# Optimization experiments

Measured on AMD Instinct MI355X. Metric: run time of the kernel, lower is better.

The kernel has to match this reference:

```python
import jax, jax.numpy as jnp
import numpy as np
import math

B, SEQ_LEN, ENC_IN = 8, 1021, 12
D_MODEL, N_HEADS, D_FF, E_LAYERS = 512, 8, 2048, 3
FACTOR, NUM_CLASS = 5, 10
BN_EPS = 1e-5


def _pos_encoding(L, d):
    pos = np.arange(L, dtype=np.float32)[:, None]
    div = np.exp(np.arange(0, d, 2, dtype=np.float32) * (-math.log(10000.0) / d))
    pe = np.zeros((L, d), dtype=np.float32)
    pe[:, 0::2] = np.sin(pos * div)
    pe[:, 1::2] = np.cos(pos * div)
    return jnp.asarray(pe)


def _layer_norm(x, w, b, eps=1e-5):
    mu = jnp.mean(x, -1, keepdims=True)
    var = jnp.mean((x - mu) ** 2, -1, keepdims=True)
    return (x - mu) * jax.lax.rsqrt(var + eps) * w + b


def _circ_conv1d(x, w, b=None):
    # x: [B,C,L], w: [O,C,3]; circular pad 1 each side then valid conv (torch padding_mode='circular')
    xp = jnp.concatenate([x[..., -1:], x, x[..., :1]], axis=-1)
    y = jax.lax.conv_general_dilated(xp, w, (1,), 'VALID', dimension_numbers=('NCH', 'OIH', 'NCH'))
    return y if b is None else y + b[None, :, None]


def _prob_attention(q, k, v, rng):
    # ProbSparse attention (mask_flag=False). q,k,v: [B,H,L,Dh]
    Bq, H, L, Dh = q.shape
    n = min(FACTOR * int(math.ceil(math.log(L))), L)      # U_part == u (L_Q == L_K)
    idx = jax.random.randint(rng, (L, n), 0, L)           # sampled key ids per query
    k_sample = k[:, :, idx, :]                            # [B,H,L,n,Dh]
    qk_sample = jnp.einsum('bhld,bhlsd->bhls', q, k_sample)
    m = qk_sample.max(-1) - qk_sample.sum(-1) / L         # sparsity measure M
    _, m_top = jax.lax.top_k(m, n)                        # [B,H,n] active queries
    q_red = jnp.take_along_axis(q, m_top[..., None], axis=2)   # [B,H,n,Dh]
    scores = jnp.einsum('bhud,bhld->bhul', q_red, k) * (1.0 / math.sqrt(Dh))
    attn = jax.nn.softmax(scores, axis=-1)
    upd = jnp.einsum('bhul,bhld->bhud', attn, v)          # [B,H,n,Dh]
    ctx = jnp.broadcast_to(jnp.mean(v, axis=2, keepdims=True), (Bq, H, L, Dh))  # initial context = mean(V)
    b_ix = jnp.arange(Bq)[:, None, None]
    h_ix = jnp.arange(H)[None, :, None]
    ctx = ctx.at[b_ix, h_ix, m_top].set(upd)
    return jnp.transpose(ctx, (0, 2, 1, 3))               # [B,L,H,Dh]


def _encoder_layer(x, l, attn_wq, attn_bq, attn_wk, attn_bk, attn_wv, attn_bv,
                   attn_wo, attn_bo, ln1_w, ln1_b, ln2_w, ln2_b,
                   ff1_w, ff1_b, ff2_w, ff2_b, rng):
    Bx, L, dm = x.shape
    Dh = dm // N_HEADS
    q = (x @ attn_wq[l].T + attn_bq[l]).reshape(Bx, L, N_HEADS, Dh).transpose(0, 2, 1, 3)
    k = (x @ attn_wk[l].T + attn_bk[l]).reshape(Bx, L, N_HEADS, Dh).transpose(0, 2, 1, 3)
    v = (x @ attn_wv[l].T + attn_bv[l]).reshape(Bx, L, N_HEADS, Dh).transpose(0, 2, 1, 3)
    ctx = _prob_attention(q, k, v, rng).reshape(Bx, L, dm)
    new_x = ctx @ attn_wo[l].T + attn_bo[l]
    x = _layer_norm(x + new_x, ln1_w[l], ln1_b[l])
    y = jax.nn.gelu(x @ ff1_w[l].T + ff1_b[l], approximate=False)
    y = y @ ff2_w[l].T + ff2_b[l]
    return _layer_norm(x + y, ln2_w[l], ln2_b[l])


def _conv_layer(x, cw, cb, bnw, bnb):
    # distillation: circular conv -> BatchNorm (eval, mean 0 / var 1) -> ELU -> MaxPool(3,2,pad=1)
    h = _circ_conv1d(jnp.transpose(x, (0, 2, 1)), cw, cb)
    h = h * (bnw * (1.0 / math.sqrt(1.0 + BN_EPS)))[None, :, None] + bnb[None, :, None]
    h = jax.nn.elu(h)
    h = jax.lax.reduce_window(h, -np.inf, jax.lax.max, (1, 1, 3), (1, 1, 2),
                              ((0, 0), (0, 0), (1, 1)))
    return jnp.transpose(h, (0, 2, 1))


def _forward(x_enc, tok_w, attn_wq, attn_bq, attn_wk, attn_bk, attn_wv, attn_bv,
             attn_wo, attn_bo, ln1_w, ln1_b, ln2_w, ln2_b, ff1_w, ff1_b, ff2_w, ff2_b,
             cv_w, cv_b, bn_w, bn_b, norm_w, norm_b, proj_w, proj_b):
    rngs = jax.random.split(jax.random.key(42), E_LAYERS)
    # DataEmbedding = TokenEmbedding (circular conv, no bias) + sinusoidal positional
    x = jnp.transpose(_circ_conv1d(jnp.transpose(x_enc, (0, 2, 1)), tok_w), (0, 2, 1))
    x = x + _pos_encoding(x.shape[1], D_MODEL)[None]
    for l in range(E_LAYERS):
        x = _encoder_layer(x, l, attn_wq, attn_bq, attn_wk, attn_bk, attn_wv, attn_bv,
                           attn_wo, attn_bo, ln1_w, ln1_b, ln2_w, ln2_b,
                           ff1_w, ff1_b, ff2_w, ff2_b, rngs[l])
        if l < E_LAYERS - 1:
            x = _conv_layer(x, cv_w[l], cv_b[l], bn_w[l], bn_b[l])
    x = _layer_norm(x, norm_w, norm_b)
    out = jax.nn.gelu(x, approximate=False)
    out = out.reshape(out.shape[0], -1)    # [B, d_model * conv_seq_len]
    return out @ proj_w.T + proj_b


def setup_inputs() -> dict:
    key = jax.random.key(0)
    ks = jax.random.split(key, 32)
    d, ff = D_MODEL, D_FF

    def nrm(k, shape, scale=1.0):
        return jax.random.normal(k, shape, dtype=jnp.float32) * scale

    s_d = 1.0 / math.sqrt(d)
    return {
        'x_enc': nrm(ks[0], (B, SEQ_LEN, ENC_IN)),
        'tok_w': nrm(ks[1], (d, ENC_IN, 3), 1.0 / math.sqrt(ENC_IN * 3)),
        'attn_wq': nrm(ks[2], (E_LAYERS, d, d), s_d), 'attn_bq': nrm(ks[3], (E_LAYERS, d), 0.02),
        'attn_wk': nrm(ks[4], (E_LAYERS, d, d), s_d), 'attn_bk': nrm(ks[5], (E_LAYERS, d), 0.02),
        'attn_wv': nrm(ks[6], (E_LAYERS, d, d), s_d), 'attn_bv': nrm(ks[7], (E_LAYERS, d), 0.02),
        'attn_wo': nrm(ks[8], (E_LAYERS, d, d), s_d), 'attn_bo': nrm(ks[9], (E_LAYERS, d), 0.02),
        'ln1_w': jnp.ones((E_LAYERS, d), jnp.float32), 'ln1_b': jnp.zeros((E_LAYERS, d), jnp.float32),
        'ln2_w': jnp.ones((E_LAYERS, d), jnp.float32), 'ln2_b': jnp.zeros((E_LAYERS, d), jnp.float32),
        'ff1_w': nrm(ks[10], (E_LAYERS, ff, d), s_d), 'ff1_b': nrm(ks[11], (E_LAYERS, ff), 0.02),
        'ff2_w': nrm(ks[12], (E_LAYERS, d, ff), 1.0 / math.sqrt(ff)), 'ff2_b': nrm(ks[13], (E_LAYERS, d), 0.02),
        'cv_w': nrm(ks[14], (E_LAYERS - 1, d, d, 3), 1.0 / math.sqrt(3 * d)),
        'cv_b': nrm(ks[15], (E_LAYERS - 1, d), 0.02),
        'bn_w': jnp.ones((E_LAYERS - 1, d), jnp.float32), 'bn_b': jnp.zeros((E_LAYERS - 1, d), jnp.float32),
        'norm_w': jnp.ones((d,), jnp.float32), 'norm_b': jnp.zeros((d,), jnp.float32),
        'proj_w': nrm(ks[16], (NUM_CLASS, d * 256), 1.0 / math.sqrt(d * 256)),
        'proj_b': jnp.zeros((NUM_CLASS,), jnp.float32),
    }


def reference(x_enc, tok_w, attn_wq, attn_bq, attn_wk, attn_bk, attn_wv, attn_bv,
              attn_wo, attn_bo, ln1_w, ln1_b, ln2_w, ln2_b, ff1_w, ff1_b, ff2_w, ff2_b,
              cv_w, cv_b, bn_w, bn_b, norm_w, norm_b, proj_w, proj_b):
    return _forward(x_enc, tok_w, attn_wq, attn_bq, attn_wk, attn_bk, attn_wv, attn_bv,
                    attn_wo, attn_bo, ln1_w, ln1_b, ln2_w, ln2_b, ff1_w, ff1_b, ff2_w, ff2_b,
                    cv_w, cv_b, bn_w, bn_b, norm_w, norm_b, proj_w, proj_b)
```

## Files before the change

kernel.cpp:

```cpp
#include <hip/hip_runtime.h>
#include <math.h>
#include <stdint.h>

typedef __attribute__((ext_vector_type(8))) short bf16x8;
typedef __attribute__((ext_vector_type(4))) float f32x4;

__device__ __forceinline__ unsigned short f2bf(float f){
  unsigned int u = __float_as_uint(f);
  unsigned int r = (u + 0x7fffu + ((u>>16)&1u)) >> 16;
  return (unsigned short)r;
}
__device__ __forceinline__ float bf2f(unsigned short h){
  return __uint_as_float(((unsigned int)h)<<16);
}
__device__ __forceinline__ void gload16(const void* g, void* l){
  __builtin_amdgcn_global_load_lds(
      (const __attribute__((address_space(1))) unsigned int*)g,
      (__attribute__((address_space(3))) unsigned int*)l, 16, 0, 0);
}

__host__ __device__ static inline uint32_t rotl32(uint32_t x, int d){ return (x<<d)|(x>>(32-d)); }
__host__ __device__ static inline void tf2x32(uint32_t k0, uint32_t k1, uint32_t c0, uint32_t c1,
                                              uint32_t* o0, uint32_t* o1){
  uint32_t ks0=k0, ks1=k1, ks2=k0^k1^0x1BD11BDAu;
  uint32_t x0=c0+ks0, x1=c1+ks1;
  const int ra[4]={13,15,26,6}, rb[4]={17,29,16,24};
  #pragma unroll
  for(int i=0;i<4;i++){x0+=x1;x1=rotl32(x1,ra[i]);x1^=x0;}
  x0+=ks1; x1+=ks2+1u;
  #pragma unroll
  for(int i=0;i<4;i++){x0+=x1;x1=rotl32(x1,rb[i]);x1^=x0;}
  x0+=ks2; x1+=ks0+2u;
  #pragma unroll
  for(int i=0;i<4;i++){x0+=x1;x1=rotl32(x1,ra[i]);x1^=x0;}
  x0+=ks0; x1+=ks1+3u;
  #pragma unroll
  for(int i=0;i<4;i++){x0+=x1;x1=rotl32(x1,rb[i]);x1^=x0;}
  x0+=ks1; x1+=ks2+4u;
  #pragma unroll
  for(int i=0;i<4;i++){x0+=x1;x1=rotl32(x1,ra[i]);x1^=x0;}
  x0+=ks2; x1+=ks0+5u;
  *o0=x0; *o1=x1;
}

__global__ __launch_bounds__(256) void gen_idx_k(uint32_t k1a,uint32_t k1b,
                                                 uint32_t k2a,uint32_t k2b,
                                                 int size,uint32_t span,uint32_t mult,
                                                 int* __restrict__ idx){
  int i = blockIdx.x*256 + threadIdx.x;
  if (i >= size) return;
  uint32_t h0,h1,l0,l1;
  tf2x32(k1a,k1b,0u,(uint32_t)i,&h0,&h1);
  tf2x32(k2a,k2b,0u,(uint32_t)i,&l0,&l1);
  uint32_t hb = h0^h1, lb = l0^l1;
  idx[i] = (int)((((hb%span)*mult) + (lb%span)) % span);
}

__global__ __launch_bounds__(256) void embed_k(const float* __restrict__ xe,
                                               const float* __restrict__ tw,
                                               float* __restrict__ X,
                                               short* __restrict__ Xh){
  int i = blockIdx.x*256 + threadIdx.x;
  int c = i & 511;
  int bl = i >> 9;
  int l = bl % 1021;
  int b = bl / 1021;
  float acc = 0.f;
  #pragma unroll
  for (int t=0;t<3;t++){
    int ls = l - 1 + t;
    ls = (ls < 0) ? 1020 : (ls >= 1021 ? 0 : ls);
    const float* xp = xe + (size_t)(b*1021 + ls)*12;
    const float* wp = tw + (size_t)c*36 + t;
    #pragma unroll
    for (int ci=0; ci<12; ci++) acc += xp[ci] * wp[ci*3];
  }
  int ip = c >> 1;
  float div = expf((float)(2*ip) * (float)(-9.210340371976184/512.0));
  float ang = (float)l * div;
  acc += (c & 1) ? cosf(ang) : sinf(ang);
  X[i] = acc;
  Xh[i] = f2bf(acc);
}

__global__ __launch_bounds__(256) void wcvt_k(const float* __restrict__ src,
                                              short* __restrict__ dst, int n){
  int i = blockIdx.x*256 + threadIdx.x;
  if (i < n) dst[i] = f2bf(src[i]);
}
__global__ __launch_bounds__(256) void convw_k(const float* __restrict__ cw,
                                               short* __restrict__ W){
  int i = blockIdx.x*256 + threadIdx.x;
  int col = i % 1536; int co = i / 1536;
  int t = col / 512; int ci = col % 512;
  W[i] = f2bf(cw[(size_t)co*1536 + ci*3 + t]);
}

__global__ __launch_bounds__(256) void gemm_bf16_k(
    const short* __restrict__ A, long Ab,
    const short* __restrict__ W, long Wb,
    const float* __restrict__ bias,
    float* __restrict__ Cf, short* __restrict__ Ch, long Cb,
    int M, int Nreal, int Nstride, int K, int mode,
    const float* __restrict__ s2, const float* __restrict__ b2,
    const float* __restrict__ rs, long rsb)
{
  __shared__ short As[4096];
  __shared__ short Bs[4096];
  const int t = threadIdx.x;
  const int lane = t & 63;
  const int w = t >> 6;
  const int wr = w >> 1, wc = w & 1;
  const int z = blockIdx.z;
  const int m0 = blockIdx.x * 128, n0 = blockIdx.y * 128;
  const short* Az = A + (size_t)z * Ab;
  const short* Wz = W + (size_t)z * Wb;

  f32x4 acc[4][4];
  #pragma unroll
  for (int i=0;i<4;i++)
    #pragma unroll
    for (int j=0;j<4;j++) acc[i][j] = (f32x4){0.f,0.f,0.f,0.f};

  const int r0  = t >> 2;
  const int k80 = (t & 3) << 3;
  char* AsB = (char*)As;
  char* BsB = (char*)Bs;

  for (int k0 = 0; k0 < K; k0 += 32){
    gload16(Az + (size_t)(m0 + r0)      * K + k0 + k80, AsB + (size_t)w*1024);
    gload16(Az + (size_t)(m0 + r0 + 64) * K + k0 + k80, AsB + 4096 + (size_t)w*1024);
    gload16(Wz + (size_t)(n0 + r0)      * K + k0 + k80, BsB + (size_t)w*1024);
    gload16(Wz + (size_t)(n0 + r0 + 64) * K + k0 + k80, BsB + 4096 + (size_t)w*1024);
    __syncthreads();
    bf16x8 a[4], b[4];
    #pragma unroll
    for (int mi=0; mi<4; mi++){
      int aoff = (wr*64 + mi*16 + (lane&15))*32 + ((lane>>4)<<3);
      a[mi] = *(const bf16x8*)(&As[aoff]);
    }
    #pragma unroll
    for (int ni=0; ni<4; ni++){
      int boff = (wc*64 + ni*16 + (lane&15))*32 + ((lane>>4)<<3);
      b[ni] = *(const bf16x8*)(&Bs[boff]);
    }
    #pragma unroll
    for (int mi=0; mi<4; mi++)
      #pragma unroll
      for (int ni=0; ni<4; ni++)
        acc[mi][ni] = __builtin_amdgcn_mfma_f32_16x16x32_bf16(a[mi], b[ni], acc[mi][ni], 0, 0, 0);
    __syncthreads();
  }

  #pragma unroll
  for (int mi=0; mi<4; mi++){
    #pragma unroll
    for (int r=0; r<4; r++){
      int gm = m0 + wr*64 + mi*16 + ((lane>>4)<<2) + r;
      if (gm >= M) continue;
      float rsc = (mode==4) ? rs[(size_t)z*rsb + gm] : 0.f;
      #pragma unroll
      for (int ni=0; ni<4; ni++){
        int gn = n0 + wc*64 + ni*16 + (lane&15);
        if (gn >= Nreal) continue;
        float v = acc[mi][ni][r];
        if (mode <= 2) v += bias[gn];
        if (mode == 1){
          v = 0.5f*v*(1.0f + erff(v*0.707106781186547524f));
        } else if (mode == 2){
          v = v * (s2[gn]*0.9999950000374997f) + b2[gn];
          v = (v > 0.f) ? v : expm1f(v);
        } else if (mode == 4){
          v *= rsc;
        }
        size_t off = (size_t)z*Cb + (size_t)gm*Nstride + gn;
        if (Cf) Cf[off] = v;
        if (Ch) Ch[off] = f2bf(v);
      }
    }
  }
}

__global__ __launch_bounds__(256) void qk_dot_k(const float* __restrict__ Q,
                                                const float* __restrict__ Kb,
                                                const int* __restrict__ idx,
                                                float* __restrict__ QK, int L, int n){
  long gi = (long)blockIdx.x*256 + threadIdx.x;
  long total = (long)64*L*n;
  if (gi >= total) return;
  int s = (int)(gi % n); long t2 = gi / n;
  int l = (int)(t2 % L); int bh = (int)(t2 / L);
  int h = bh & 7, b = bh >> 3;
  const float4* qp = (const float4*)(Q + (size_t)(b*L + l)*512 + h*64);
  int kr = idx[l*n + s];
  const float4* kp = (const float4*)(Kb + (size_t)(b*L + kr)*512 + h*64);
  float dot = 0.f;
  #pragma unroll
  for (int i=0;i<16;i++){
    float4 a = qp[i], c = kp[i];
    dot += a.x*c.x + a.y*c.y + a.z*c.z + a.w*c.w;
  }
  QK[gi] = dot;
}

__global__ __launch_bounds__(256) void reduce_m_k(const float* __restrict__ QK,
                                                  float* __restrict__ Mout, int L, int n){
  int gi = blockIdx.x*256 + threadIdx.x;
  if (gi >= 64*L) return;
  int l = gi % L; int bh = gi / L;
  const float* row = QK + (size_t)gi*n;
  float mx = -INFINITY, sm = 0.f;
  for (int s=0;s<n;s++){ float v = row[s]; mx = fmaxf(mx, v); sm += v; }
  Mout[(size_t)bh*1024 + l] = mx - sm/(float)L;
}

__global__ __launch_bounds__(64) void topk_k(const float* __restrict__ Mv,
                                             int* __restrict__ topk, int L, int n){
  int bh = blockIdx.x; int lane = threadIdx.x;
  float v[16];
  #pragma unroll
  for (int i=0;i<16;i++){ int l = i*64 + lane; v[i] = (l<L) ? Mv[(size_t)bh*1024 + l] : -INFINITY; }
  for (int it=0; it<n; ++it){
    float bv = -INFINITY; int bi = 0x7fffffff;
    #pragma unroll
    for (int i=0;i<16;i++){ int l = i*64+lane; if (v[i] > bv){ bv = v[i]; bi = l; } }
    #pragma unroll
    for (int o=32;o>0;o>>=1){
      float ov = __shfl_xor(bv, o); int oi = __shfl_xor(bi, o);
      if (ov > bv || (ov == bv && oi < bi)){ bv = ov; bi = oi; }
    }
    if (lane == 0) topk[bh*n + it] = bi;
    int wl = bi & 63, wi = bi >> 6;
    if (lane == wl){
      #pragma unroll
      for (int i=0;i<16;i++) if (i == wi) v[i] = -INFINITY;
    }
  }
}

__global__ __launch_bounds__(64) void qred_k(const float* __restrict__ Q,
                                             const int* __restrict__ topk,
                                             short* __restrict__ Qrh, int L, int n){
  int u = blockIdx.x % n; int bh = blockIdx.x / n;
  int h = bh & 7, b = bh >> 3; int d = threadIdx.x;
  int lq = topk[bh*n + u];
  Qrh[(size_t)bh*8192 + u*64 + d] = f2bf(0.125f * Q[(size_t)(b*L + lq)*512 + h*64 + d]);
}

__global__ __launch_bounds__(256) void kh_k(const float* __restrict__ Kb,
                                            short* __restrict__ Kh, int L){
  int i = blockIdx.x*256 + threadIdx.x;
  int d = i & 63; int l = (i>>6) & 1023; int bh = i >> 16;
  int h = bh & 7, b = bh >> 3;
  Kh[i] = (l < L) ? f2bf(Kb[(size_t)(b*L + l)*512 + h*64 + d]) : (short)0;
}

__global__ __launch_bounds__(256) void vt_k(const float* __restrict__ V,
                                            short* __restrict__ Vt, int L){
  __shared__ float ts[64][65];
  int z = blockIdx.x >> 4;
  int l0 = (blockIdx.x & 15) * 64;
  int h = z & 7, b = z >> 3;
  int t = threadIdx.x;
  for (int i = t; i < 4096; i += 256){
    int lloc = i >> 6, d = i & 63;
    int l = l0 + lloc;
    ts[d][lloc] = (l < L) ? V[(size_t)(b*L + l)*512 + h*64 + d] : 0.f;
  }
  __syncthreads();
  for (int i = t; i < 4096; i += 256){
    int d = i >> 6, lloc = i & 63;
    Vt[(size_t)z*131072 + (size_t)d*1024 + l0 + lloc] = f2bf(ts[d][lloc]);
  }
}

__global__ __launch_bounds__(256) void softmax_k(const float* __restrict__ S,
                                                 short* __restrict__ Ph,
                                                 float* __restrict__ RS, int L, int n){
  int u = blockIdx.x % n; int z = blockIdx.x / n;
  const float* srow = S + (size_t)z*n*1024 + (size_t)u*1024;
  short* prow = Ph + (size_t)z*131072 + (size_t)u*1024;
  int t = threadIdx.x;
  __shared__ float red[256];
  float lm = -INFINITY;
  for (int l=t; l<L; l+=256) lm = fmaxf(lm, srow[l]);
  red[t]=lm; __syncthreads();
  for (int o=128;o>0;o>>=1){ if(t<o) red[t]=fmaxf(red[t],red[t+o]); __syncthreads(); }
  float mx = red[0]; __syncthreads();
  float ls = 0.f;
  for (int l=t; l<1024; l+=256){
    float p = (l < L) ? expf(srow[l]-mx) : 0.f;
    prow[l] = f2bf(p);
    ls += p;
  }
  red[t]=ls; __syncthreads();
  for (int o=128;o>0;o>>=1){ if(t<o) red[t]+=red[t+o]; __syncthreads(); }
  if (t==0) RS[(size_t)z*n + u] = 1.0f/red[0];
}

__global__ __launch_bounds__(512) void vmean_part_k(const float* __restrict__ V,
                                                    float* __restrict__ part, int L){
  int b = blockIdx.x; int j = blockIdx.y; int c = threadIdx.x;
  float s = 0.f;
  for (int l = j; l < L; l += 16) s += V[(size_t)(b*L + l)*512 + c];
  part[(size_t)(b*16 + j)*512 + c] = s;
}
__global__ __launch_bounds__(256) void vmean_comb_k(const float* __restrict__ part,
                                                    float* __restrict__ vmean, int L){
  int i = blockIdx.x*256 + threadIdx.x;
  int b = i >> 9; int c = i & 511;
  float s = 0.f;
  #pragma unroll
  for (int j=0;j<16;j++) s += part[(size_t)(b*16 + j)*512 + c];
  vmean[i] = s / (float)L;
}
__global__ __launch_bounds__(256) void ctx_fill_k(short* __restrict__ CTXh,
                                                  const float* __restrict__ vmean, int L){
  int i = blockIdx.x*256 + threadIdx.x;
  int c = i & 511; int bl = i >> 9; int b = bl / L;
  CTXh[i] = f2bf(vmean[b*512 + c]);
}
__global__ __launch_bounds__(256) void ctx_scatter_k(short* __restrict__ CTXh,
                                                     const float* __restrict__ UPD,
                                                     const int* __restrict__ topk, int L, int n){
  int i = blockIdx.x*256 + threadIdx.x;
  int d = i & 63; int u = (i >> 6) % n; int bh = i / (64*n);
  int h = bh & 7; int b = bh >> 3;
  int lq = topk[bh*n + u];
  CTXh[(size_t)(b*L + lq)*512 + h*64 + d] = f2bf(UPD[((size_t)bh*n + u)*64 + d]);
}

__global__ __launch_bounds__(256) void add_ln_k(float* __restrict__ X,
                                                short* __restrict__ Xh,
                                                const float* __restrict__ Y,
                                                const float* __restrict__ w,
                                                const float* __restrict__ b){
  int r = blockIdx.x;
  size_t base = (size_t)r*512;
  int t = threadIdx.x;
  float v0 = X[base+t]     + Y[base+t];
  float v1 = X[base+t+256] + Y[base+t+256];
  __shared__ float red[256];
  red[t] = v0 + v1; __syncthreads();
  for (int o=128;o>0;o>>=1){ if(t<o) red[t]+=red[t+o]; __syncthreads(); }
  float mu = red[0]*(1.f/512.f); __syncthreads();
  float d0 = v0-mu, d1 = v1-mu;
  red[t] = d0*d0 + d1*d1; __syncthreads();
  for (int o=128;o>0;o>>=1){ if(t<o) red[t]+=red[t+o]; __syncthreads(); }
  float rs = 1.0f/sqrtf(red[0]*(1.f/512.f) + 1e-5f);
  float x0 = d0*rs*w[t]     + b[t];
  float x1 = d1*rs*w[t+256] + b[t+256];
  X[base+t]     = x0;  Xh[base+t]     = f2bf(x0);
  X[base+t+256] = x1;  Xh[base+t+256] = f2bf(x1);
}

__global__ __launch_bounds__(256) void ln_gelu_k(const float* __restrict__ X,
                                                 float* __restrict__ Yout,
                                                 const float* __restrict__ w,
                                                 const float* __restrict__ b){
  int r = blockIdx.x;
  size_t base = (size_t)r*512;
  int t = threadIdx.x;
  float v0 = X[base+t];
  float v1 = X[base+t+256];
  __shared__ float red[256];
  red[t] = v0 + v1; __syncthreads();
  for (int o=128;o>0;o>>=1){ if(t<o) red[t]+=red[t+o]; __syncthreads(); }
  float mu = red[0]*(1.f/512.f); __syncthreads();
  float d0 = v0-mu, d1 = v1-mu;
  red[t] = d0*d0 + d1*d1; __syncthreads();
  for (int o=128;o>0;o>>=1){ if(t<o) red[t]+=red[t+o]; __syncthreads(); }
  float rs = 1.0f/sqrtf(red[0]*(1.f/512.f) + 1e-5f);
  float g0 = d0*rs*w[t]     + b[t];
  float g1 = d1*rs*w[t+256] + b[t+256];
  Yout[base+t]     = 0.5f*g0*(1.0f + erff(g0*0.707106781186547524f));
  Yout[base+t+256] = 0.5f*g1*(1.0f + erff(g1*0.707106781186547524f));
}

__global__ __launch_bounds__(256) void im2col_k(const float* __restrict__ X,
                                                short* __restrict__ O, int L){
  int i = blockIdx.x*256 + threadIdx.x;
  int col = i % 1536; int bl = i / 1536;
  int l = bl % L; int b = bl / L;
  int t = col / 512; int ci = col % 512;
  int ls = l - 1 + t;
  ls = (ls < 0) ? (L-1) : (ls >= L ? 0 : ls);
  O[(size_t)bl*1536 + col] = f2bf(X[(size_t)(b*L + ls)*512 + ci]);
}
__global__ __launch_bounds__(256) void pool_k(const short* __restrict__ Hc,
                                              float* __restrict__ X,
                                              short* __restrict__ Xh, int L, int Lo){
  int i = blockIdx.x*256 + threadIdx.x;
  int c = i & 511; int r = i >> 9; int lo = r % Lo; int b = r / Lo;
  float m = -INFINITY;
  #pragma unroll
  for (int dt=-1; dt<=1; dt++){
    int li = 2*lo + dt;
    if (li >= 0 && li < L) m = fmaxf(m, bf2f((unsigned short)Hc[(size_t)(b*L + li)*512 + c]));
  }
  size_t o = (size_t)(b*Lo + lo)*512 + c;
  X[o] = m; Xh[o] = f2bf(m);
}

__global__ __launch_bounds__(256) void proj_part_k(const float* __restrict__ Xg,
                                                   const float* __restrict__ pw,
                                                   float* __restrict__ part){
  int b = blockIdx.x >> 5;
  int c = blockIdx.x & 31;
  int t = threadIdx.x;
  const float4* xp = (const float4*)(Xg + (size_t)b*131072 + (size_t)c*4096);
  float4 x0 = xp[t], x1 = xp[t+256], x2 = xp[t+512], x3 = xp[t+768];
  float acc[10];
  #pragma unroll
  for (int j=0;j<10;j++){
    const float4* wp = (const float4*)(pw + (size_t)j*131072 + (size_t)c*4096);
    float4 w0 = wp[t], w1 = wp[t+256], w2 = wp[t+512], w3 = wp[t+768];
    acc[j] = x0.x*w0.x + x0.y*w0.y + x0.z*w0.z + x0.w*w0.w
           + x1.x*w1.x + x1.y*w1.y + x1.z*w1.z + x1.w*w1.w
           + x2.x*w2.x + x2.y*w2.y + x2.z*w2.z + x2.w*w2.w
           + x3.x*w3.x + x3.y*w3.y + x3.z*w3.z + x3.w*w3.w;
  }
  __shared__ float red[256];
  #pragma unroll
  for (int j=0;j<10;j++){
    red[t] = acc[j]; __syncthreads();
    for (int o=128;o>0;o>>=1){ if(t<o) red[t]+=red[t+o]; __syncthreads(); }
    if (t==0) part[(b*10 + j)*32 + c] = red[0];
    __syncthreads();
  }
}
__global__ __launch_bounds__(128) void proj_comb_k(const float* __restrict__ part,
                                                   const float* __restrict__ pb,
                                                   float* __restrict__ out){
  int t = threadIdx.x;
  if (t >= 80) return;
  int j = t % 10;
  const float* p = part + t*32;
  float s = 0.f;
  #pragma unroll
  for (int c=0;c<32;c++) s += p[c];
  out[t] = s + pb[j];
}

extern "C" void kernel_launch(void* const* d_in, const int* in_sizes, int n_in,
                              void* d_out, int out_size, void* d_ws, size_t ws_size,
                              hipStream_t stream){
  (void)in_sizes; (void)n_in; (void)out_size; (void)ws_size;
  const float* x_enc = (const float*)d_in[0];
  const float* tok_w = (const float*)d_in[1];
  const float* wq    = (const float*)d_in[2];
  const float* bq    = (const float*)d_in[3];
  const float* wk    = (const float*)d_in[4];
  const float* bk    = (const float*)d_in[5];
  const float* wvp   = (const float*)d_in[6];
  const float* bvp   = (const float*)d_in[7];
  const float* wo    = (const float*)d_in[8];
  const float* bo    = (const float*)d_in[9];
  const float* ln1w  = (const float*)d_in[10];
  const float* ln1b  = (const float*)d_in[11];
  const float* ln2w  = (const float*)d_in[12];
  const float* ln2b  = (const float*)d_in[13];
  const float* f1w   = (const float*)d_in[14];
  const float* f1b   = (const float*)d_in[15];
  const float* f2w   = (const float*)d_in[16];
  const float* f2b   = (const float*)d_in[17];
  const float* cvw   = (const float*)d_in[18];
  const float* cvb   = (const float*)d_in[19];
  const float* bnw   = (const float*)d_in[20];
  const float* bnb   = (const float*)d_in[21];
  const float* nw    = (const float*)d_in[22];
  const float* nb    = (const float*)d_in[23];
  const float* pw    = (const float*)d_in[24];
  const float* pb    = (const float*)d_in[25];

  char* wsb = (char*)d_ws;
  float* X    = (float*)(wsb + 0);
  float* Y    = (float*)(wsb + 16777216);
  float* Q    = (float*)(wsb + 33554432);
  float* Kbuf = (float*)(wsb + 50331648);
  float* V    = (float*)(wsb + 67108864);
  short* Xh   = (short*)(wsb + 83886080);
  short* CTXh = (short*)(wsb + 92274688);
  short* WQH  = (short*)(wsb + 100663296);
  short* WKH  = WQH + 262144;
  short* WVH  = WKH + 262144;
  short* WOH  = WVH + 262144;
  short* F1H  = WOH + 262144;
  short* F2H  = F1H + 1048576;
  short* WCVH = F2H + 1048576;
  char*  RB   = wsb + 108527616;
  short* FFh  = (short*)(RB);
  short* IM2  = (short*)(RB + 33554432);
  short* Kh   = (short*)(RB + 0);
  short* Vt   = (short*)(RB + 8388608);
  short* Ph   = (short*)(RB + 25165824);
  short* Qrh  = (short*)(RB + 41943040);
  float* S    = (float*)(RB + 42991616);
  float* RS   = (float*)(RB + 52166656);
  float* UPD  = (float*)(RB + 52175616);
  float* Mb   = (float*)(RB + 52749056);
  float* VME  = (float*)(RB + 53011200);
  float* VPA  = (float*)(RB + 53027584);
  int*   IDX  = (int*)  (RB + 53289728);
  int*   TOPK = (int*)  (RB + 53433088);
  float* PPART= (float*)(RB + 53450752);

  uint32_t rka[3], rkb[3];
  for (int l = 0; l < 3; ++l) tf2x32(0u, 42u, 0u, (uint32_t)l, &rka[l], &rkb[l]);

  auto gemm = [&](const short* A, long Ab, const short* W, long Wb, const float* bias,
                  float* Cf, short* Ch, long Cb, int M, int Nreal, int Nstride, int K,
                  int mode, const float* s2, const float* b2, const float* rs, long rsb,
                  int mt, int nt, int zt){
    hipLaunchKernelGGL(gemm_bf16_k, dim3(mt, nt, zt), dim3(256), 0, stream,
                       A, Ab, W, Wb, bias, Cf, Ch, Cb, M, Nreal, Nstride, K, mode,
                       s2, b2, rs, rsb);
  };

  hipLaunchKernelGGL(embed_k, dim3(16336), dim3(256), 0, stream, x_enc, tok_w, X, Xh);

  int L = 1021;
  for (int l = 0; l < 3; ++l){
    int n = 5 * (int)ceil(log((double)L)); if (n > L) n = L;
    int Mr = 8 * L;
    int mt = (Mr + 127)/128;

    hipLaunchKernelGGL(wcvt_k, dim3(1024), dim3(256), 0, stream, wq + (size_t)l*262144, WQH, 262144);
    hipLaunchKernelGGL(wcvt_k, dim3(1024), dim3(256), 0, stream, wk + (size_t)l*262144, WKH, 262144);
    hipLaunchKernelGGL(wcvt_k, dim3(1024), dim3(256), 0, stream, wvp+ (size_t)l*262144, WVH, 262144);
    hipLaunchKernelGGL(wcvt_k, dim3(1024), dim3(256), 0, stream, wo + (size_t)l*262144, WOH, 262144);
    hipLaunchKernelGGL(wcvt_k, dim3(4096), dim3(256), 0, stream, f1w+ (size_t)l*1048576, F1H, 1048576);
    hipLaunchKernelGGL(wcvt_k, dim3(4096), dim3(256), 0, stream, f2w+ (size_t)l*1048576, F2H, 1048576);

    uint32_t k1a,k1b,k2a,k2b;
    tf2x32(rka[l], rkb[l], 0u, 0u, &k1a, &k1b);
    tf2x32(rka[l], rkb[l], 0u, 1u, &k2a, &k2b);
    int size = L * n;
    uint32_t span = (uint32_t)L;
    uint32_t rr = 65536u % span;
    uint32_t mult = (rr * rr) % span;
    hipLaunchKernelGGL(gen_idx_k, dim3((unsigned)((size+255)/256)), dim3(256), 0, stream,
                       k1a, k1b, k2a, k2b, size, span, mult, IDX);

    gemm(Xh, 0, WQH, 0, bq + (size_t)l*512, Q,    nullptr, 0, Mr, 512, 512, 512, 0, 0, 0, 0, 0, mt, 4, 1);
    gemm(Xh, 0, WKH, 0, bk + (size_t)l*512, Kbuf, nullptr, 0, Mr, 512, 512, 512, 0, 0, 0, 0, 0, mt, 4, 1);
    gemm(Xh, 0, WVH, 0, bvp+ (size_t)l*512, V,    nullptr, 0, Mr, 512, 512, 512, 0, 0, 0, 0, 0, mt, 4, 1);

    long tot = (long)64*L*n;
    hipLaunchKernelGGL(qk_dot_k, dim3((unsigned)((tot+255)/256)), dim3(256), 0, stream,
                       Q, Kbuf, IDX, S, L, n);
    hipLaunchKernelGGL(reduce_m_k, dim3((unsigned)((64*L+255)/256)), dim3(256), 0, stream,
                       S, Mb, L, n);
    hipLaunchKernelGGL(topk_k, dim3(64), dim3(64), 0, stream, Mb, TOPK, L, n);

    hipLaunchKernelGGL(qred_k, dim3((unsigned)(64*n)), dim3(64), 0, stream, Q, TOPK, Qrh, L, n);
    hipLaunchKernelGGL(kh_k, dim3(16384), dim3(256), 0, stream, Kbuf, Kh, L);
    hipLaunchKernelGGL(vt_k, dim3(1024), dim3(256), 0, stream, V, Vt, L);
    gemm(Qrh, 8192, Kh, 65536, nullptr, S, nullptr, (long)n*1024, n, L, 1024, 64, 3, 0, 0, 0, 0, 1, 8, 64);
    hipLaunchKernelGGL(softmax_k, dim3((unsigned)(64*n)), dim3(256), 0, stream, S, Ph, RS, L, n);
    gemm(Ph, 131072, Vt, 131072, nullptr, UPD, nullptr, (long)n*64, n, 64, 64, 1024, 4, 0, 0, RS, n, 1, 1, 64);

    hipLaunchKernelGGL(vmean_part_k, dim3(8,16), dim3(512), 0, stream, V, VPA, L);
    hipLaunchKernelGGL(vmean_comb_k, dim3(16), dim3(256), 0, stream, VPA, VME, L);
    hipLaunchKernelGGL(ctx_fill_k, dim3((unsigned)(Mr*2)), dim3(256), 0, stream, CTXh, VME, L);
    hipLaunchKernelGGL(ctx_scatter_k, dim3((unsigned)(16*n)), dim3(256), 0, stream, CTXh, UPD, TOPK, L, n);

    gemm(CTXh, 0, WOH, 0, bo + (size_t)l*512, Y, nullptr, 0, Mr, 512, 512, 512, 0, 0, 0, 0, 0, mt, 4, 1);
    hipLaunchKernelGGL(add_ln_k, dim3((unsigned)Mr), dim3(256), 0, stream, X, Xh, Y, ln1w + (size_t)l*512, ln1b + (size_t)l*512);

    gemm(Xh, 0, F1H, 0, f1b + (size_t)l*2048, nullptr, FFh, 0, Mr, 2048, 2048, 512, 1, 0, 0, 0, 0, mt, 16, 1);
    gemm(FFh, 0, F2H, 0, f2b + (size_t)l*512, Y, nullptr, 0, Mr, 512, 512, 2048, 0, 0, 0, 0, 0, mt, 4, 1);
    hipLaunchKernelGGL(add_ln_k, dim3((unsigned)Mr), dim3(256), 0, stream, X, Xh, Y, ln2w + (size_t)l*512, ln2b + (size_t)l*512);

    if (l < 2){
      hipLaunchKernelGGL(convw_k, dim3(3072), dim3(256), 0, stream, cvw + (size_t)l*786432, WCVH);
      hipLaunchKernelGGL(im2col_k, dim3((unsigned)(Mr*6)), dim3(256), 0, stream, X, IM2, L);
      gemm(IM2, 0, WCVH, 0, cvb + (size_t)l*512, nullptr, CTXh, 0, Mr, 512, 512, 1536, 2,
           bnw + (size_t)l*512, bnb + (size_t)l*512, 0, 0, mt, 4, 1);
      int Lo = (L - 1)/2 + 1;
      hipLaunchKernelGGL(pool_k, dim3((unsigned)(8*Lo*2)), dim3(256), 0, stream, CTXh, X, Xh, L, Lo);
      L = Lo;
    }
  }

  hipLaunchKernelGGL(ln_gelu_k, dim3((unsigned)(8*L)), dim3(256), 0, stream, X, Y, nw, nb);
  hipLaunchKernelGGL(proj_part_k, dim3(256), dim3(256), 0, stream, Y, pw, PPART);
  hipLaunchKernelGGL(proj_comb_k, dim3(1), dim3(128), 0, stream, PPART, pb, (float*)d_out);
}
```

Measured before the change: 1.714 ms.

## Double-buffer GEMM LDS tiles, fuse K head-layout write, restructure sampled QK dot

The bf16 GEMM now double-buffers its LDS tiles, issuing the next k-slice's global-to-LDS loads before the MFMAs on the current slice. This is meant to hide load latency, and it costs twice the shared memory. The K projection GEMM epilogue now also writes the per-head bf16 K layout directly, so the separate kh_k conversion kernel is dropped. That kernel used to zero the padded rows, and those rows are now left unwritten. The sampled QK kernel now uses one block per (batch, query), staging the query row in LDS once and sharing it across all heads and samples instead of rereading it per thread.

```diff
diff --git a/kernel.cpp b/kernel.cpp
--- a/kernel.cpp
+++ b/kernel.cpp
@@ -103,10 +103,11 @@
     float* __restrict__ Cf, short* __restrict__ Ch, long Cb,
     int M, int Nreal, int Nstride, int K, int mode,
     const float* __restrict__ s2, const float* __restrict__ b2,
-    const float* __restrict__ rs, long rsb)
+    const float* __restrict__ rs, long rsb,
+    short* __restrict__ KhG, int Lq)
 {
-  __shared__ short As[4096];
-  __shared__ short Bs[4096];
+  __shared__ short As[8192];
+  __shared__ short Bs[8192];
   const int t = threadIdx.x;
   const int lane = t & 63;
   const int w = t >> 6;
@@ -127,21 +128,27 @@
   char* AsB = (char*)As;
   char* BsB = (char*)Bs;
 
+  #define STAGE(buf, k0) do { \
+    gload16(Az + (size_t)(m0 + r0)      * K + (k0) + k80, AsB + (buf)*8192 + (size_t)w*1024); \
+    gload16(Az + (size_t)(m0 + r0 + 64) * K + (k0) + k80, AsB + (buf)*8192 + 4096 + (size_t)w*1024); \
+    gload16(Wz + (size_t)(n0 + r0)      * K + (k0) + k80, BsB + (buf)*8192 + (size_t)w*1024); \
+    gload16(Wz + (size_t)(n0 + r0 + 64) * K + (k0) + k80, BsB + (buf)*8192 + 4096 + (size_t)w*1024); \
+  } while(0)
+
+  STAGE(0, 0);
+  __syncthreads();
+  int cur = 0;
   for (int k0 = 0; k0 < K; k0 += 32){
-    gload16(Az + (size_t)(m0 + r0)      * K + k0 + k80, AsB + (size_t)w*1024);
-    gload16(Az + (size_t)(m0 + r0 + 64) * K + k0 + k80, AsB + 4096 + (size_t)w*1024);
-    gload16(Wz + (size_t)(n0 + r0)      * K + k0 + k80, BsB + (size_t)w*1024);
-    gload16(Wz + (size_t)(n0 + r0 + 64) * K + k0 + k80, BsB + 4096 + (size_t)w*1024);
-    __syncthreads();
+    if (k0 + 32 < K) STAGE(cur^1, k0+32);
     bf16x8 a[4], b[4];
     #pragma unroll
     for (int mi=0; mi<4; mi++){
-      int aoff = (wr*64 + mi*16 + (lane&15))*32 + ((lane>>4)<<3);
+      int aoff = cur*4096 + (wr*64 + mi*16 + (lane&15))*32 + ((lane>>4)<<3);
       a[mi] = *(const bf16x8*)(&As[aoff]);
     }
     #pragma unroll
     for (int ni=0; ni<4; ni++){
-      int boff = (wc*64 + ni*16 + (lane&15))*32 + ((lane>>4)<<3);
+      int boff = cur*4096 + (wc*64 + ni*16 + (lane&15))*32 + ((lane>>4)<<3);
       b[ni] = *(const bf16x8*)(&Bs[boff]);
     }
     #pragma unroll
@@ -150,7 +157,9 @@
       for (int ni=0; ni<4; ni++)
         acc[mi][ni] = __builtin_amdgcn_mfma_f32_16x16x32_bf16(a[mi], b[ni], acc[mi][ni], 0, 0, 0);
     __syncthreads();
-  }
+    cur ^= 1;
+  }
+  #undef STAGE
 
   #pragma unroll
   for (int mi=0; mi<4; mi++){
@@ -159,6 +168,8 @@
       int gm = m0 + wr*64 + mi*16 + ((lane>>4)<<2) + r;
       if (gm >= M) continue;
       float rsc = (mode==4) ? rs[(size_t)z*rsb + gm] : 0.f;
+      int bb = 0, ll = 0;
+      if (KhG){ bb = gm / Lq; ll = gm - bb*Lq; }
       #pragma unroll
       for (int ni=0; ni<4; ni++){
         int gn = n0 + wc*64 + ni*16 + (lane&15);
@@ -176,31 +187,37 @@
         size_t off = (size_t)z*Cb + (size_t)gm*Nstride + gn;
         if (Cf) Cf[off] = v;
         if (Ch) Ch[off] = f2bf(v);
+        if (KhG) KhG[(((size_t)bb*8 + (gn>>6))*1024 + ll)*64 + (gn&63)] = f2bf(v);
       }
     }
   }
 }
 
-__global__ __launch_bounds__(256) void qk_dot_k(const float* __restrict__ Q,
+__global__ __launch_bounds__(320) void qk_dot_k(const float* __restrict__ Q,
                                                 const float* __restrict__ Kb,
                                                 const int* __restrict__ idx,
                                                 float* __restrict__ QK, int L, int n){
-  long gi = (long)blockIdx.x*256 + threadIdx.x;
-  long total = (long)64*L*n;
-  if (gi >= total) return;
-  int s = (int)(gi % n); long t2 = gi / n;
-  int l = (int)(t2 % L); int bh = (int)(t2 / L);
-  int h = bh & 7, b = bh >> 3;
-  const float4* qp = (const float4*)(Q + (size_t)(b*L + l)*512 + h*64);
-  int kr = idx[l*n + s];
-  const float4* kp = (const float4*)(Kb + (size_t)(b*L + kr)*512 + h*64);
-  float dot = 0.f;
-  #pragma unroll
-  for (int i=0;i<16;i++){
-    float4 a = qp[i], c = kp[i];
-    dot += a.x*c.x + a.y*c.y + a.z*c.z + a.w*c.w;
-  }
-  QK[gi] = dot;
+  __shared__ float Qs[512];
+  int blk = blockIdx.x;
+  int l = blk % L, b = blk / L;
+  int t = threadIdx.x;
+  if (t < 128){
+    gload16(Q + (size_t)(b*L + l)*512 + t*4, (char*)Qs + (size_t)(t>>6)*1024);
+  }
+  __syncthreads();
+  if (t < 8*n){
+    int h = t / n, s = t - h*n;
+    int kr = idx[l*n + s];
+    const float4* kp = (const float4*)(Kb + (size_t)(b*L + kr)*512 + h*64);
+    const float4* qp = (const float4*)(Qs + h*64);
+    float dot = 0.f;
+    #pragma unroll
+    for (int i=0;i<16;i++){
+      float4 a = qp[i], c = kp[i];
+      dot += a.x*c.x + a.y*c.y + a.z*c.z + a.w*c.w;
+    }
+    QK[((size_t)(b*8 + h)*L + l)*n + s] = dot;
+  }
 }
 
 __global__ __launch_bounds__(256) void reduce_m_k(const float* __restrict__ QK,
@@ -245,14 +262,6 @@
   int h = bh & 7, b = bh >> 3; int d = threadIdx.x;
   int lq = topk[bh*n + u];
   Qrh[(size_t)bh*8192 + u*64 + d] = f2bf(0.125f * Q[(size_t)(b*L + lq)*512 + h*64 + d]);
-}
-
-__global__ __launch_bounds__(256) void kh_k(const float* __restrict__ Kb,
-                                            short* __restrict__ Kh, int L){
-  int i = blockIdx.x*256 + threadIdx.x;
-  int d = i & 63; int l = (i>>6) & 1023; int bh = i >> 16;
-  int h = bh & 7, b = bh >> 3;
-  Kh[i] = (l < L) ? f2bf(Kb[(size_t)(b*L + l)*512 + h*64 + d]) : (short)0;
 }
 
 __global__ __launch_bounds__(256) void vt_k(const float* __restrict__ V,
@@ -511,10 +520,10 @@
   auto gemm = [&](const short* A, long Ab, const short* W, long Wb, const float* bias,
                   float* Cf, short* Ch, long Cb, int M, int Nreal, int Nstride, int K,
                   int mode, const float* s2, const float* b2, const float* rs, long rsb,
-                  int mt, int nt, int zt){
+                  int mt, int nt, int zt, short* KhG, int Lq){
     hipLaunchKernelGGL(gemm_bf16_k, dim3(mt, nt, zt), dim3(256), 0, stream,
                        A, Ab, W, Wb, bias, Cf, Ch, Cb, M, Nreal, Nstride, K, mode,
-                       s2, b2, rs, rsb);
+                       s2, b2, rs, rsb, KhG, Lq);
   };
 
   hipLaunchKernelGGL(embed_k, dim3(16336), dim3(256), 0, stream, x_enc, tok_w, X, Xh);
@@ -542,41 +551,39 @@
     hipLaunchKernelGGL(gen_idx_k, dim3((unsigned)((size+255)/256)), dim3(256), 0, stream,
                        k1a, k1b, k2a, k2b, size, span, mult, IDX);
 
-    gemm(Xh, 0, WQH, 0, bq + (size_t)l*512, Q,    nullptr, 0, Mr, 512, 512, 512, 0, 0, 0, 0, 0, mt, 4, 1);
-    gemm(Xh, 0, WKH, 0, bk + (size_t)l*512, Kbuf, nullptr, 0, Mr, 512, 512, 512, 0, 0, 0, 0, 0, mt, 4, 1);
-    gemm(Xh, 0, WVH, 0, bvp+ (size_t)l*512, V,    nullptr, 0, Mr, 512, 512, 512, 0, 0, 0, 0, 0, mt, 4, 1);
-
-    long tot = (long)64*L*n;
-    hipLaunchKernelGGL(qk_dot_k, dim3((unsigned)((tot+255)/256)), dim3(256), 0, stream,
+    gemm(Xh, 0, WQH, 0, bq + (size_t)l*512, Q,    nullptr, 0, Mr, 512, 512, 512, 0, 0, 0, 0, 0, mt, 4, 1, nullptr, 0);
+    gemm(Xh, 0, WKH, 0, bk + (size_t)l*512, Kbuf, nullptr, 0, Mr, 512, 512, 512, 0, 0, 0, 0, 0, mt, 4, 1, Kh, L);
+    gemm(Xh, 0, WVH, 0, bvp+ (size_t)l*512, V,    nullptr, 0, Mr, 512, 512, 512, 0, 0, 0, 0, 0, mt, 4, 1, nullptr, 0);
+
+    hipLaunchKernelGGL(qk_dot_k, dim3((unsigned)(8*L)), dim3(320), 0, stream,
                        Q, Kbuf, IDX, S, L, n);
     hipLaunchKernelGGL(reduce_m_k, dim3((unsigned)((64*L+255)/256)), dim3(256), 0, stream,
                        S, Mb, L, n);
     hipLaunchKernelGGL(topk_k, dim3(64), dim3(64), 0, stream, Mb, TOPK, L, n);
 
     hipLaunchKernelGGL(qred_k, dim3((unsigned)(64*n)), dim3(64), 0, stream, Q, TOPK, Qrh, L, n);
-    hipLaunchKernelGGL(kh_k, dim3(16384), dim3(256), 0, stream, Kbuf, Kh, L);
     hipLaunchKernelGGL(vt_k, dim3(1024), dim3(256), 0, stream, V, Vt, L);
-    gemm(Qrh, 8192, Kh, 65536, nullptr, S, nullptr, (long)n*1024, n, L, 1024, 64, 3, 0, 0, 0, 0, 1, 8, 64);
+    gemm(Qrh, 8192, Kh, 65536, nullptr, S, nullptr, (long)n*1024, n, L, 1024, 64, 3, 0, 0, 0, 0, 1, 8, 64, nullptr, 0);
     hipLaunchKernelGGL(softmax_k, dim3((unsigned)(64*n)), dim3(256), 0, stream, S, Ph, RS, L, n);
-    gemm(Ph, 131072, Vt, 131072, nullptr, UPD, nullptr, (long)n*64, n, 64, 64, 1024, 4, 0, 0, RS, n, 1, 1, 64);
+    gemm(Ph, 131072, Vt, 131072, nullptr, UPD, nullptr, (long)n*64, n, 64, 64, 1024, 4, 0, 0, RS, n, 1, 1, 64, nullptr, 0);
 
     hipLaunchKernelGGL(vmean_part_k, dim3(8,16), dim3(512), 0, stream, V, VPA, L);
     hipLaunchKernelGGL(vmean_comb_k, dim3(16), dim3(256), 0, stream, VPA, VME, L);
     hipLaunchKernelGGL(ctx_fill_k, dim3((unsigned)(Mr*2)), dim3(256), 0, stream, CTXh, VME, L);
     hipLaunchKernelGGL(ctx_scatter_k, dim3((unsigned)(16*n)), dim3(256), 0, stream, CTXh, UPD, TOPK, L, n);
 
-    gemm(CTXh, 0, WOH, 0, bo + (size_t)l*512, Y, nullptr, 0, Mr, 512, 512, 512, 0, 0, 0, 0, 0, mt, 4, 1);
+    gemm(CTXh, 0, WOH, 0, bo + (size_t)l*512, Y, nullptr, 0, Mr, 512, 512, 512, 0, 0, 0, 0, 0, mt, 4, 1, nullptr, 0);
     hipLaunchKernelGGL(add_ln_k, dim3((unsigned)Mr), dim3(256), 0, stream, X, Xh, Y, ln1w + (size_t)l*512, ln1b + (size_t)l*512);
 
-    gemm(Xh, 0, F1H, 0, f1b + (size_t)l*2048, nullptr, FFh, 0, Mr, 2048, 2048, 512, 1, 0, 0, 0, 0, mt, 16, 1);
-    gemm(FFh, 0, F2H, 0, f2b + (size_t)l*512, Y, nullptr, 0, Mr, 512, 512, 2048, 0, 0, 0, 0, 0, mt, 4, 1);
+    gemm(Xh, 0, F1H, 0, f1b + (size_t)l*2048, nullptr, FFh, 0, Mr, 2048, 2048, 512, 1, 0, 0, 0, 0, mt, 16, 1, nullptr, 0);
+    gemm(FFh, 0, F2H, 0, f2b + (size_t)l*512, Y, nullptr, 0, Mr, 512, 512, 2048, 0, 0, 0, 0, 0, mt, 4, 1, nullptr, 0);
     hipLaunchKernelGGL(add_ln_k, dim3((unsigned)Mr), dim3(256), 0, stream, X, Xh, Y, ln2w + (size_t)l*512, ln2b + (size_t)l*512);
 
     if (l < 2){
       hipLaunchKernelGGL(convw_k, dim3(3072), dim3(256), 0, stream, cvw + (size_t)l*786432, WCVH);
       hipLaunchKernelGGL(im2col_k, dim3((unsigned)(Mr*6)), dim3(256), 0, stream, X, IM2, L);
       gemm(IM2, 0, WCVH, 0, cvb + (size_t)l*512, nullptr, CTXh, 0, Mr, 512, 512, 1536, 2,
-           bnw + (size_t)l*512, bnb + (size_t)l*512, 0, 0, mt, 4, 1);
+           bnw + (size_t)l*512, bnb + (size_t)l*512, 0, 0, mt, 4, 1, nullptr, 0);
       int Lo = (L - 1)/2 + 1;
       hipLaunchKernelGGL(pool_k, dim3((unsigned)(8*Lo*2)), dim3(256), 0, stream, CTXh, X, Xh, L, Lo);
       L = Lo;
```

New measurement: 1.685 ms. About the same (-1.7%).
